# Kernel tuning notes

Measured on AMD Instinct MI355X. Metric: run time of the kernel, lower is better.

## Reference

```python
import jax, jax.numpy as jnp
import numpy as np
import math

EMBED_DIMS = 256
NUM_LANDMARKS = 40  # hard-coded k=40 in the original module
B, N = 2, 8192


def setup_inputs() -> dict:
    key = jax.random.key(0)
    ks = jax.random.split(key, 9)
    C = EMBED_DIMS
    w = lambda k: jax.random.normal(k, (C, C), dtype=jnp.float32) * 0.02
    b = lambda k: jax.random.normal(k, (C,), dtype=jnp.float32) * 0.02
    return {
        "query": jax.random.normal(ks[0], (B, N, C), dtype=jnp.float32),
        "Wq": w(ks[1]), "bq": b(ks[2]),
        "Wk": w(ks[3]), "bk": b(ks[4]),
        "Wv": w(ks[5]), "bv": b(ks[6]),
        "Wo": w(ks[7]), "bo": b(ks[8]),
    }


def reference(query, Wq, bq, Wk, bk, Wv, bv, Wo, bo):
    # key = value = identity = query (defaults in the original forward)
    C = query.shape[-1]
    scaling = math.sqrt(C)

    q = query @ Wq.T + bq  # [B, N, C]
    k = query @ Wk.T + bk
    v = query @ Wv.T + bv

    # Full similarity only to score keys: score_m[b, m] = sum_n sim_nm[b, n, m]
    sim_nm = jnp.einsum('bnc,bmc->bnm', q, k) / scaling  # [B, N, N]
    score_m = sim_nm.sum(axis=1)                          # [B, N]

    _, top_idx = jax.lax.top_k(score_m, NUM_LANDMARKS)    # [B, 40]
    selected = jnp.take_along_axis(k, top_idx[:, :, None], axis=1)  # [B, 40, C]

    sim_qn = jax.nn.softmax(jnp.einsum('bnc,bkc->bnk', q, selected) / scaling, axis=-1)  # [B, N, 40]
    sim_km = jax.nn.softmax(jnp.einsum('bmc,bkc->bmk', k, selected) / scaling, axis=-1)  # [B, N, 40]

    sim_qk = jnp.einsum('bnk,bmk->bnm', sim_qn, sim_km)   # [B, N, N]
    out = jnp.einsum('bnm,bmc->bnc', sim_qk, v)           # [B, N, C]
    out = out @ Wo.T + bo
    return query + out  # identity residual; dropouts are identity at p=0
```

## Files before the change

kernel.cpp:

```cpp
#include <hip/hip_runtime.h>
#include <cstddef>
#include <cstdint>

#define BATCH 2
#define SEQ 8192
#define CH 256
#define NLM 40
#define NLMP 48
#define MROWS (BATCH * SEQ)
#define INV_SCALE 0.0625f
#define NCBLK 256

typedef unsigned short ushort_t;
typedef __attribute__((ext_vector_type(8))) short short8;
typedef __attribute__((ext_vector_type(4))) float floatx4;

__device__ __forceinline__ ushort_t f2bf(float f) {
    unsigned int u = __float_as_uint(f);
    u += 0x7FFFu + ((u >> 16) & 1u);
    return (ushort_t)(u >> 16);
}
__device__ __forceinline__ float bf2f(ushort_t u) {
    return __uint_as_float(((unsigned)u) << 16);
}

__device__ __forceinline__ void gload_lds16(const ushort_t* g, ushort_t* l) {
    __builtin_amdgcn_global_load_lds(
        (const __attribute__((address_space(1))) unsigned int*)g,
        (__attribute__((address_space(3))) unsigned int*)l, 16, 0, 0);
}

__global__ __launch_bounds__(256) void convert_colsum(const float* __restrict__ x,
                                                      ushort_t* __restrict__ xbf,
                                                      float* __restrict__ partial) {
    __shared__ float red[4][256];
    const int b = blockIdx.y;
    const int r0 = blockIdx.x * 32;
    const int t = threadIdx.x;
    const int c4 = (t & 63) * 4;
    const int rg = t >> 6;
    const float* base = x + ((size_t)b * SEQ + r0) * 256;
    ushort_t* obase = xbf + ((size_t)b * SEQ + r0) * 256;
    float4 s = {0.f, 0.f, 0.f, 0.f};
#pragma unroll
    for (int i = 0; i < 8; i++) {
        const int r = rg + i * 4;
        const float4 a = *(const float4*)&base[(size_t)r * 256 + c4];
        uint2 o;
        o.x = f2bf(a.x) | ((unsigned)f2bf(a.y) << 16);
        o.y = f2bf(a.z) | ((unsigned)f2bf(a.w) << 16);
        *(uint2*)&obase[(size_t)r * 256 + c4] = o;
        s.x += a.x; s.y += a.y; s.z += a.z; s.w += a.w;
    }
    *(float4*)&red[rg][c4] = s;
    __syncthreads();
    const float tot = red[0][t] + red[1][t] + red[2][t] + red[3][t];
    partial[((size_t)b * NCBLK + blockIdx.x) * 256 + t] = tot;
}

__global__ __launch_bounds__(1024) void ws_kernel(const float* __restrict__ partial,
                                                  const float* __restrict__ Wq,
                                                  const float* __restrict__ bq,
                                                  const float* __restrict__ Wk,
                                                  float* __restrict__ ws,
                                                  float* __restrict__ tmat) {
    const int b = blockIdx.x;
    __shared__ float xs[256];
    __shared__ float qs[256];
    __shared__ float ppart[4][256];
    const int t = threadIdx.x;
    {
        float* tz = tmat + (size_t)b * NLM * 256;
        for (int i = t; i < NLM * 256; i += 1024) tz[i] = 0.f;
    }
    {
        const int c = t & 255, qd = t >> 8;
        const float* pb = partial + ((size_t)b * NCBLK + qd * 64) * 256 + c;
        float a = 0.f;
#pragma unroll 8
        for (int i = 0; i < 64; i++) a += pb[(size_t)i * 256];
        ppart[qd][c] = a;
    }
    __syncthreads();
    if (t < 256) xs[t] = ppart[0][t] + ppart[1][t] + ppart[2][t] + ppart[3][t];
    __syncthreads();
    const int lane = t & 63, w = t >> 6;
    {
        float4 wq[16];
#pragma unroll
        for (int g = 0; g < 16; g++)
            wq[g] = *(const float4*)&Wq[(size_t)(w * 16 + g) * 256 + lane * 4];
        const float4 x4 = *(const float4*)&xs[lane * 4];
#pragma unroll
        for (int g = 0; g < 16; g++) {
            const int o = w * 16 + g;
            float d = wq[g].x * x4.x + wq[g].y * x4.y + wq[g].z * x4.z + wq[g].w * x4.w;
#pragma unroll
            for (int off = 32; off >= 1; off >>= 1) d += __shfl_down(d, off);
            if (lane == 0) qs[o] = d + 8192.0f * bq[o];
        }
    }
    __syncthreads();
    const int c = t & 255, part = t >> 8;
    float a = 0.f;
#pragma unroll 16
    for (int o = part * 64; o < part * 64 + 64; o++)
        a += Wk[(size_t)o * 256 + c] * qs[o];
    ppart[part][c] = a;
    __syncthreads();
    if (t < 256)
        ws[b * 256 + t] = ppart[0][t] + ppart[1][t] + ppart[2][t] + ppart[3][t];
}

__global__ __launch_bounds__(256) void gemm_qkv_score(const ushort_t* __restrict__ xbf,
                                                      const float* __restrict__ Wq,
                                                      const float* __restrict__ Wk,
                                                      const float* __restrict__ Wv,
                                                      const float* __restrict__ bq,
                                                      const float* __restrict__ bk,
                                                      const float* __restrict__ bv,
                                                      ushort_t* __restrict__ qkv,
                                                      const float* __restrict__ query,
                                                      const float* __restrict__ ws,
                                                      float* __restrict__ score) {
    __shared__ __align__(16) char smem[24576];
    ushort_t* As = (ushort_t*)smem;
    ushort_t* Bs = (ushort_t*)(smem + 16384);
    ushort_t* Es = (ushort_t*)smem;
    const int z = blockIdx.z;
    const int t = threadIdx.x;
    const int lane = t & 63;
    const int w = t >> 6;

    if (z == 3) {
        const int blk = blockIdx.y * 4 + blockIdx.x;
#pragma unroll
        for (int i = 0; i < 8; i++) {
            const int g = blk * 32 + i * 4 + w;
            const int b = g >> 13;
            const int m = g & 8191;
            const float4 kv = *(const float4*)&query[(size_t)g * 256 + lane * 4];
            const float4 qs = *(const float4*)&ws[b * 256 + lane * 4];
            float d = kv.x * qs.x + kv.y * qs.y + kv.z * qs.z + kv.w * qs.w;
#pragma unroll
            for (int off = 32; off >= 1; off >>= 1) d += __shfl_down(d, off);
            if (lane == 0) score[(size_t)b * SEQ + m] = d * INV_SCALE;
        }
        return;
    }

    const float* __restrict__ W = (z == 0) ? Wq : (z == 1) ? Wk : Wv;
    const float* __restrict__ bias = (z == 0) ? bq : (z == 1) ? bk : bv;
    ushort_t* __restrict__ out = qkv + (size_t)z * MROWS * 256;
    const int o0 = blockIdx.x * 64;
    const int m0 = blockIdx.y * 128;
    const int quad = lane >> 4;
    const int l16 = lane & 15;
    const int xsw = l16 & 7;

    floatx4 acc[2][4];
#pragma unroll
    for (int rt = 0; rt < 2; rt++)
#pragma unroll
        for (int ct = 0; ct < 4; ct++) acc[rt][ct] = (floatx4){0.f, 0.f, 0.f, 0.f};

    for (int kc = 0; kc < 256; kc += 64) {
#pragma unroll
        for (int q = 0; q < 4; q++) {
            const int r0 = w * 32 + q * 8;
            gload_lds16(&xbf[(size_t)(m0 + r0 + (lane >> 3)) * 256 + kc +
                             (((lane & 7) ^ (lane >> 3)) * 8)],
                        &As[r0 * 64]);
        }
#pragma unroll
        for (int u = 0; u < 2; u++) {
            const int cid = t + u * 256;
            const int row = cid >> 3;
            const int cch = cid & 7;
            const float* wp = &W[(size_t)(o0 + row) * 256 + kc + cch * 8];
            const float4 a = *(const float4*)wp;
            const float4 c = *(const float4*)(wp + 4);
            uint4 o;
            o.x = f2bf(a.x) | ((unsigned)f2bf(a.y) << 16);
            o.y = f2bf(a.z) | ((unsigned)f2bf(a.w) << 16);
            o.z = f2bf(c.x) | ((unsigned)f2bf(c.y) << 16);
            o.w = f2bf(c.z) | ((unsigned)f2bf(c.w) << 16);
            *(uint4*)&Bs[row * 64 + ((cch ^ (row & 7)) * 8)] = o;
        }
        __syncthreads();
#pragma unroll
        for (int s = 0; s < 2; s++) {
            short8 a[2], bf[4];
#pragma unroll
            for (int rt = 0; rt < 2; rt++)
                a[rt] = *(const short8*)&As[(w * 32 + rt * 16 + l16) * 64 +
                                            (((s * 4 + quad) ^ xsw) * 8)];
#pragma unroll
            for (int ct = 0; ct < 4; ct++)
                bf[ct] = *(const short8*)&Bs[(ct * 16 + l16) * 64 +
                                             (((s * 4 + quad) ^ xsw) * 8)];
#pragma unroll
            for (int rt = 0; rt < 2; rt++)
#pragma unroll
                for (int ct = 0; ct < 4; ct++)
                    acc[rt][ct] = __builtin_amdgcn_mfma_f32_16x16x32_bf16(
                        a[rt], bf[ct], acc[rt][ct], 0, 0, 0);
        }
        __syncthreads();
    }

#pragma unroll
    for (int rt = 0; rt < 2; rt++) {
#pragma unroll
        for (int ct = 0; ct < 4; ct++) {
            const int col = ct * 16 + l16;
            const float bb = bias[o0 + col];
#pragma unroll
            for (int reg = 0; reg < 4; reg++) {
                const int row = w * 32 + rt * 16 + quad * 4 + reg;
                Es[row * 72 + col] = f2bf(acc[rt][ct][reg] + bb);
            }
        }
    }
    __syncthreads();
#pragma unroll
    for (int u = 0; u < 4; u++) {
        const int cid = t + u * 256;
        const int row = cid >> 3;
        const int off = (cid & 7) * 8;
        *(uint4*)&out[(size_t)(m0 + row) * 256 + o0 + off] =
            *(const uint4*)&Es[row * 72 + off];
    }
}

__global__ __launch_bounds__(1024) void topk_gather(const float* __restrict__ score,
                                                    const ushort_t* __restrict__ kmat,
                                                    ushort_t* __restrict__ sel) {
    const int b = blockIdx.x;
    const int t = threadIdx.x;
    __shared__ unsigned hist[256];
    __shared__ unsigned wsum[64];
    __shared__ unsigned sPrefix, sMask, sRem, sNeq;
    __shared__ int sNgt;
    __shared__ int top[NLM];
    __shared__ unsigned topkey[NLM];

    unsigned key[8];
#pragma unroll
    for (int j = 0; j < 8; j++) {
        const unsigned u = __float_as_uint(score[(size_t)b * SEQ + t + j * 1024]);
        key[j] = u ^ (unsigned)(((int)u >> 31) | 0x80000000);
    }
    if (t == 0) { sPrefix = 0; sMask = 0; sRem = NLM; sNgt = 0; sNeq = 0; }

    for (int lvl = 0; lvl < 4; lvl++) {
        const int shift = 24 - 8 * lvl;
        if (t < 256) hist[t] = 0;
        __syncthreads();
        const unsigned pfx = sPrefix, msk = sMask;
#pragma unroll
        for (int j = 0; j < 8; j++)
            if (((key[j] ^ pfx) & msk) == 0)
                atomicAdd(&hist[(key[j] >> shift) & 255u], 1u);
        __syncthreads();
        if (t < 64) wsum[t] = hist[t * 4] + hist[t * 4 + 1] + hist[t * 4 + 2] + hist[t * 4 + 3];
        __syncthreads();
        if (t == 0) {
            unsigned rem = sRem, cum = 0;
            int g = 63;
            for (; g > 0; g--) { if (cum + wsum[g] >= rem) break; cum += wsum[g]; }
            int d = g * 4 + 3;
            for (; d > g * 4; d--) { if (cum + hist[d] >= rem) break; cum += hist[d]; }
            sRem = rem - cum;
            sPrefix |= ((unsigned)d) << shift;
            sMask |= 255u << shift;
        }
        __syncthreads();
    }
    const unsigned K40 = sPrefix;
    const unsigned rem = sRem;
    const int ngt = NLM - (int)rem;

#pragma unroll
    for (int j = 0; j < 8; j++) {
        if (key[j] > K40) {
            const int slot = atomicAdd(&sNgt, 1);
            top[slot] = t + j * 1024; topkey[slot] = key[j];
        } else if (key[j] == K40) {
            const unsigned e = atomicAdd(&sNeq, 1u);
            if (e < rem) {
                const int slot = ngt + (int)e;
                top[slot] = t + j * 1024; topkey[slot] = key[j];
            }
        }
    }
    __syncthreads();

    if (t < 64) {
        unsigned long long c = (t < NLM)
            ? ((((unsigned long long)(~topkey[t])) << 32) | (unsigned)top[t])
            : 0xFFFFFFFFFFFFFFFFull;
#pragma unroll
        for (int kk = 2; kk <= 64; kk <<= 1) {
#pragma unroll
            for (int j = kk >> 1; j >= 1; j >>= 1) {
                const unsigned long long o = __shfl_xor(c, j);
                const bool takeMin = ((t & kk) == 0) == ((t & j) == 0);
                const bool less = c < o;
                c = (takeMin == less) ? c : o;
            }
        }
        if (t < NLM) top[t] = (int)(c & 0xFFFFFFFFu);
    }
    __syncthreads();

    for (int f = t; f < NLMP * 256; f += 1024) {
        const int j = f >> 8;
        const int cc = f & 255;
        sel[(size_t)b * NLMP * 256 + f] =
            (j < NLM) ? kmat[((size_t)b * SEQ + top[j]) * 256 + cc] : (ushort_t)0;
    }
}

__global__ __launch_bounds__(256, 4) void sim_fused(const ushort_t* __restrict__ qbf,
                                                    const ushort_t* __restrict__ kbf,
                                                    const ushort_t* __restrict__ vbf,
                                                    const ushort_t* __restrict__ sel,
                                                    float* __restrict__ simq,
                                                    float* __restrict__ tmat) {
    __shared__ __align__(16) char smem[43008];
    float (*Ps)[40]  = (float(*)[40])smem;
    ushort_t* Vs     = (ushort_t*)(smem + 10240);
    const int b = blockIdx.y;
    const int n0 = blockIdx.x * 64;
    const int t = threadIdx.x;
    const int lane = t & 63;
    const int w = t >> 6;
    const int quad = lane >> 4;
    const int l16 = lane & 15;
    const ushort_t* __restrict__ A = (blockIdx.z == 0) ? qbf : kbf;
    const ushort_t* __restrict__ Arow = A + ((size_t)b * SEQ + n0 + w * 16 + l16) * 256;
    const ushort_t* __restrict__ Sb = sel + (size_t)b * NLMP * 256 + (size_t)l16 * 256;

    floatx4 acc[3];
#pragma unroll
    for (int ct = 0; ct < 3; ct++) acc[ct] = (floatx4){0.f, 0.f, 0.f, 0.f};

#pragma unroll
    for (int ks = 0; ks < 8; ks++) {
        const int ko = ks * 32 + quad * 8;
        const short8 a  = *(const short8*)&Arow[ko];
        const short8 b0 = *(const short8*)&Sb[ko];
        const short8 b1 = *(const short8*)&Sb[16 * 256 + ko];
        const short8 b2 = *(const short8*)&Sb[32 * 256 + ko];
        acc[0] = __builtin_amdgcn_mfma_f32_16x16x32_bf16(a, b0, acc[0], 0, 0, 0);
        acc[1] = __builtin_amdgcn_mfma_f32_16x16x32_bf16(a, b1, acc[1], 0, 0, 0);
        acc[2] = __builtin_amdgcn_mfma_f32_16x16x32_bf16(a, b2, acc[2], 0, 0, 0);
    }

    const bool v2ok = (l16 < 8);
    float p0[4], p1[4], p2[4];
#pragma unroll
    for (int reg = 0; reg < 4; reg++) {
        const float l0 = acc[0][reg] * INV_SCALE;
        const float l1 = acc[1][reg] * INV_SCALE;
        const float l2 = acc[2][reg] * INV_SCALE;
        float m = fmaxf(l0, l1);
        if (v2ok) m = fmaxf(m, l2);
        m = fmaxf(m, __shfl_xor(m, 1));
        m = fmaxf(m, __shfl_xor(m, 2));
        m = fmaxf(m, __shfl_xor(m, 4));
        m = fmaxf(m, __shfl_xor(m, 8));
        const float e0 = expf(l0 - m);
        const float e1 = expf(l1 - m);
        const float e2 = v2ok ? expf(l2 - m) : 0.f;
        float s = e0 + e1 + e2;
        s += __shfl_xor(s, 1);
        s += __shfl_xor(s, 2);
        s += __shfl_xor(s, 4);
        s += __shfl_xor(s, 8);
        const float inv = 1.f / s;
        p0[reg] = e0 * inv; p1[reg] = e1 * inv; p2[reg] = e2 * inv;
    }

    const int row0 = w * 16 + quad * 4;
    if (blockIdx.z == 0) {
        float* __restrict__ dst = &simq[((size_t)b * SEQ + n0 + row0) * NLM];
#pragma unroll
        for (int reg = 0; reg < 4; reg++) {
            float* __restrict__ d2 = dst + reg * NLM;
            d2[l16] = p0[reg];
            d2[16 + l16] = p1[reg];
            if (v2ok) d2[32 + l16] = p2[reg];
        }
        return;
    }

#pragma unroll
    for (int reg = 0; reg < 4; reg++) {
        Ps[row0 + reg][l16] = p0[reg];
        Ps[row0 + reg][16 + l16] = p1[reg];
        if (v2ok) Ps[row0 + reg][32 + l16] = p2[reg];
    }
#pragma unroll
    for (int u = 0; u < 8; u++) {
        gload_lds16(&vbf[((size_t)b * SEQ + n0 + w * 2 + u * 8 + (lane >> 5)) * 256 +
                         (lane & 31) * 8],
                    &Vs[(w * 2 + u * 8) * 256]);
    }
    __syncthreads();

    float tac[40];
#pragma unroll
    for (int j = 0; j < 40; j++) tac[j] = 0.f;

#pragma unroll 2
    for (int m = 0; m < 64; m++) {
        const float vv = bf2f(Vs[m * 256 + t]);
#pragma unroll
        for (int j4 = 0; j4 < 10; j4++) {
            const float4 p = *(const float4*)&Ps[m][j4 * 4];
            tac[j4 * 4 + 0] = fmaf(p.x, vv, tac[j4 * 4 + 0]);
            tac[j4 * 4 + 1] = fmaf(p.y, vv, tac[j4 * 4 + 1]);
            tac[j4 * 4 + 2] = fmaf(p.z, vv, tac[j4 * 4 + 2]);
            tac[j4 * 4 + 3] = fmaf(p.w, vv, tac[j4 * 4 + 3]);
        }
    }
#pragma unroll
    for (int j = 0; j < 40; j++)
        atomicAdd(&tmat[(size_t)b * NLM * 256 + j * 256 + t], tac[j]);
}

__global__ __launch_bounds__(256) void out_pre_kernel(const float* __restrict__ simq,
                                                      const float* __restrict__ tmat,
                                                      ushort_t* __restrict__ outp_bf) {
    __shared__ float Pm[64][40];
    const int g0 = blockIdx.x * 64;
    const int b = g0 >> 13;
    const int t = threadIdx.x;
    float* pflat = &Pm[0][0];
    for (int f = t; f < 64 * NLM; f += 256) pflat[f] = simq[(size_t)g0 * NLM + f];
    float tc[40];
#pragma unroll
    for (int l = 0; l < 40; l++) tc[l] = tmat[(size_t)b * NLM * 256 + l * 256 + t];
    __syncthreads();
#pragma unroll 2
    for (int m = 0; m < 64; m++) {
        float a = 0.f;
#pragma unroll
        for (int j4 = 0; j4 < 10; j4++) {
            const float4 p = *(const float4*)&Pm[m][j4 * 4];
            a = fmaf(p.x, tc[j4 * 4 + 0], a);
            a = fmaf(p.y, tc[j4 * 4 + 1], a);
            a = fmaf(p.z, tc[j4 * 4 + 2], a);
            a = fmaf(p.w, tc[j4 * 4 + 3], a);
        }
        outp_bf[((size_t)g0 + m) * 256 + t] = f2bf(a);
    }
}

__global__ __launch_bounds__(256) void gemm_out(const ushort_t* __restrict__ Abf,
                                                const float* __restrict__ Wo,
                                                const float* __restrict__ bias,
                                                const float* __restrict__ resid,
                                                float* __restrict__ out) {
    __shared__ __align__(16) char smem[34816];
    ushort_t* As = (ushort_t*)smem;
    ushort_t* Bs = (ushort_t*)(smem + 16384);
    float* Ft = (float*)smem;
    const int t = threadIdx.x;
    const int o0 = blockIdx.x * 64;
    const int m0 = blockIdx.y * 128;
    const int lane = t & 63;
    const int w = t >> 6;
    const int quad = lane >> 4;
    const int l16 = lane & 15;
    const int xsw = l16 & 7;

    floatx4 acc[2][4];
#pragma unroll
    for (int rt = 0; rt < 2; rt++)
#pragma unroll
        for (int ct = 0; ct < 4; ct++) acc[rt][ct] = (floatx4){0.f, 0.f, 0.f, 0.f};

    for (int kc = 0; kc < 256; kc += 64) {
#pragma unroll
        for (int q = 0; q < 4; q++) {
            const int r0 = w * 32 + q * 8;
            gload_lds16(&Abf[(size_t)(m0 + r0 + (lane >> 3)) * 256 + kc +
                             (((lane & 7) ^ (lane >> 3)) * 8)],
                        &As[r0 * 64]);
        }
#pragma unroll
        for (int u = 0; u < 2; u++) {
            const int cid = t + u * 256;
            const int row = cid >> 3;
            const int cch = cid & 7;
            const float* wp = &Wo[(size_t)(o0 + row) * 256 + kc + cch * 8];
            const float4 a = *(const float4*)wp;
            const float4 c = *(const float4*)(wp + 4);
            uint4 o;
            o.x = f2bf(a.x) | ((unsigned)f2bf(a.y) << 16);
            o.y = f2bf(a.z) | ((unsigned)f2bf(a.w) << 16);
            o.z = f2bf(c.x) | ((unsigned)f2bf(c.y) << 16);
            o.w = f2bf(c.z) | ((unsigned)f2bf(c.w) << 16);
            *(uint4*)&Bs[row * 64 + ((cch ^ (row & 7)) * 8)] = o;
        }
        __syncthreads();
#pragma unroll
        for (int s = 0; s < 2; s++) {
            short8 a[2], bf[4];
#pragma unroll
            for (int rt = 0; rt < 2; rt++)
                a[rt] = *(const short8*)&As[(w * 32 + rt * 16 + l16) * 64 +
                                            (((s * 4 + quad) ^ xsw) * 8)];
#pragma unroll
            for (int ct = 0; ct < 4; ct++)
                bf[ct] = *(const short8*)&Bs[(ct * 16 + l16) * 64 +
                                             (((s * 4 + quad) ^ xsw) * 8)];
#pragma unroll
            for (int rt = 0; rt < 2; rt++)
#pragma unroll
                for (int ct = 0; ct < 4; ct++)
                    acc[rt][ct] = __builtin_amdgcn_mfma_f32_16x16x32_bf16(
                        a[rt], bf[ct], acc[rt][ct], 0, 0, 0);
        }
        __syncthreads();
    }

#pragma unroll
    for (int rt = 0; rt < 2; rt++) {
#pragma unroll
        for (int ct = 0; ct < 4; ct++) {
            const int col = ct * 16 + l16;
            const float bb = bias[o0 + col];
#pragma unroll
            for (int reg = 0; reg < 4; reg++) {
                const int row = w * 32 + rt * 16 + quad * 4 + reg;
                Ft[row * 68 + col] = acc[rt][ct][reg] + bb;
            }
        }
    }
    __syncthreads();
#pragma unroll
    for (int u = 0; u < 8; u++) {
        const int cid = t + u * 256;
        const int row = cid >> 4;
        const int off = (cid & 15) * 4;
        const float4 v = *(const float4*)&Ft[row * 68 + off];
        const float4 r4 = *(const float4*)&resid[(size_t)(m0 + row) * 256 + o0 + off];
        float4 o;
        o.x = v.x + r4.x; o.y = v.y + r4.y; o.z = v.z + r4.z; o.w = v.w + r4.w;
        *(float4*)&out[(size_t)(m0 + row) * 256 + o0 + off] = o;
    }
}

extern "C" void kernel_launch(void* const* d_in, const int* in_sizes, int n_in,
                              void* d_out, int out_size, void* d_ws, size_t ws_size,
                              hipStream_t stream) {
    const float* query = (const float*)d_in[0];
    const float* Wq = (const float*)d_in[1];
    const float* bq = (const float*)d_in[2];
    const float* Wk = (const float*)d_in[3];
    const float* bk = (const float*)d_in[4];
    const float* Wv = (const float*)d_in[5];
    const float* bv = (const float*)d_in[6];
    const float* Wo = (const float*)d_in[7];
    const float* bo = (const float*)d_in[8];
    float* out = (float*)d_out;

    char* p = (char*)d_ws;
    float* simq  = (float*)p;            p += (size_t)MROWS * NLM * 4;
    ushort_t* selbf = (ushort_t*)p;      p += (size_t)BATCH * NLMP * 256 * 2;
    float* tmat  = (float*)p;            p += (size_t)BATCH * NLM * 256 * 4;
    float* partial = (float*)p;          p += (size_t)BATCH * NCBLK * 256 * 4;
    float* ws    = (float*)p;            p += (size_t)BATCH * 256 * 4;
    float* score = (float*)p;            p += (size_t)BATCH * SEQ * 4;
    ushort_t* qkv = (ushort_t*)p;        p += (size_t)3 * MROWS * 256 * 2;
    ushort_t* xbf = (ushort_t*)p;        p += (size_t)MROWS * 256 * 2;
    ushort_t* qbf = qkv;
    ushort_t* kbf = qkv + (size_t)MROWS * 256;
    ushort_t* vbf = qkv + (size_t)2 * MROWS * 256;
    ushort_t* outp_bf = xbf;

    const dim3 blk(256);

    convert_colsum<<<dim3(SEQ / 32, BATCH), blk, 0, stream>>>(query, xbf, partial);
    ws_kernel<<<dim3(BATCH), dim3(1024), 0, stream>>>(partial, Wq, bq, Wk, ws, tmat);

    gemm_qkv_score<<<dim3(4, MROWS / 128, 4), blk, 0, stream>>>(
        xbf, Wq, Wk, Wv, bq, bk, bv, qkv, query, ws, score);

    topk_gather<<<dim3(BATCH), dim3(1024), 0, stream>>>(score, kbf, selbf);

    sim_fused<<<dim3(SEQ / 64, BATCH, 2), blk, 0, stream>>>(qbf, kbf, vbf, selbf, simq, tmat);

    out_pre_kernel<<<dim3(MROWS / 64), blk, 0, stream>>>(simq, tmat, outp_bf);
    gemm_out<<<dim3(4, MROWS / 128), blk, 0, stream>>>(outp_bf, Wo, bo, query, out);
}
```

Measured before the change: 188.1 us.

## Fuse out_pre into output GEMM and remap QKV grid for XCD locality

Merges the simq×tmat product into the output projection kernel, so the bf16 intermediate is built in shared memory per 64-row tile and is never written to or reread from global memory. Each 512-thread block covers all 256 output columns, which means the full Wo is converted to bf16 in every block. It also flattens the QKV GEMM grid to 1D with a remap that interleaves blocks across the 8 XCDs, aiming for better L2 locality. The costs are redundant Wo conversion per block, an epilogue that writes scattered non-vectorized stores, and tmat recompute per k-chunk.

New measurement: 185.2 us. No clear change (-1.6%).

```diff
diff --git a/kernel.cpp b/kernel.cpp
--- a/kernel.cpp
+++ b/kernel.cpp
@@ -127,13 +127,17 @@
     ushort_t* As = (ushort_t*)smem;
     ushort_t* Bs = (ushort_t*)(smem + 16384);
     ushort_t* Es = (ushort_t*)smem;
-    const int z = blockIdx.z;
+    const int lin = blockIdx.x;
+    const int wg = (lin & 7) * 256 + (lin >> 3);
+    const int bx = wg & 3;
+    const int by = (wg >> 2) & 127;
+    const int z = wg >> 9;
     const int t = threadIdx.x;
     const int lane = t & 63;
     const int w = t >> 6;
 
     if (z == 3) {
-        const int blk = blockIdx.y * 4 + blockIdx.x;
+        const int blk = by * 4 + bx;
 #pragma unroll
         for (int i = 0; i < 8; i++) {
             const int g = blk * 32 + i * 4 + w;
@@ -152,8 +156,8 @@
     const float* __restrict__ W = (z == 0) ? Wq : (z == 1) ? Wk : Wv;
     const float* __restrict__ bias = (z == 0) ? bq : (z == 1) ? bk : bv;
     ushort_t* __restrict__ out = qkv + (size_t)z * MROWS * 256;
-    const int o0 = blockIdx.x * 64;
-    const int m0 = blockIdx.y * 128;
+    const int o0 = bx * 64;
+    const int m0 = by * 128;
     const int quad = lane >> 4;
     const int l16 = lane & 15;
     const int xsw = l16 & 7;
@@ -431,72 +435,65 @@
         atomicAdd(&tmat[(size_t)b * NLM * 256 + j * 256 + t], tac[j]);
 }
 
-__global__ __launch_bounds__(256) void out_pre_kernel(const float* __restrict__ simq,
-                                                      const float* __restrict__ tmat,
-                                                      ushort_t* __restrict__ outp_bf) {
-    __shared__ float Pm[64][40];
-    const int g0 = blockIdx.x * 64;
-    const int b = g0 >> 13;
+__global__ __launch_bounds__(512) void out_fused(const float* __restrict__ simq,
+                                                 const float* __restrict__ tmat,
+                                                 const float* __restrict__ Wo,
+                                                 const float* __restrict__ bias,
+                                                 const float* __restrict__ resid,
+                                                 float* __restrict__ out) {
+    __shared__ __align__(16) char smem[51200];
+    float* Ps = (float*)smem;
+    ushort_t* Ac = (ushort_t*)(smem + 10240);
+    ushort_t* Bs = (ushort_t*)(smem + 18432);
+
     const int t = threadIdx.x;
-    float* pflat = &Pm[0][0];
-    for (int f = t; f < 64 * NLM; f += 256) pflat[f] = simq[(size_t)g0 * NLM + f];
-    float tc[40];
-#pragma unroll
-    for (int l = 0; l < 40; l++) tc[l] = tmat[(size_t)b * NLM * 256 + l * 256 + t];
-    __syncthreads();
-#pragma unroll 2
-    for (int m = 0; m < 64; m++) {
-        float a = 0.f;
-#pragma unroll
-        for (int j4 = 0; j4 < 10; j4++) {
-            const float4 p = *(const float4*)&Pm[m][j4 * 4];
-            a = fmaf(p.x, tc[j4 * 4 + 0], a);
-            a = fmaf(p.y, tc[j4 * 4 + 1], a);
-            a = fmaf(p.z, tc[j4 * 4 + 2], a);
-            a = fmaf(p.w, tc[j4 * 4 + 3], a);
-        }
-        outp_bf[((size_t)g0 + m) * 256 + t] = f2bf(a);
-    }
-}
-
-__global__ __launch_bounds__(256) void gemm_out(const ushort_t* __restrict__ Abf,
-                                                const float* __restrict__ Wo,
-                                                const float* __restrict__ bias,
-                                                const float* __restrict__ resid,
-                                                float* __restrict__ out) {
-    __shared__ __align__(16) char smem[34816];
-    ushort_t* As = (ushort_t*)smem;
-    ushort_t* Bs = (ushort_t*)(smem + 16384);
-    float* Ft = (float*)smem;
-    const int t = threadIdx.x;
-    const int o0 = blockIdx.x * 64;
-    const int m0 = blockIdx.y * 128;
+    const int m0 = blockIdx.x * 64;
+    const int b = blockIdx.x >> 7;
     const int lane = t & 63;
     const int w = t >> 6;
     const int quad = lane >> 4;
     const int l16 = lane & 15;
     const int xsw = l16 & 7;
-
-    floatx4 acc[2][4];
-#pragma unroll
-    for (int rt = 0; rt < 2; rt++)
-#pragma unroll
-        for (int ct = 0; ct < 4; ct++) acc[rt][ct] = (floatx4){0.f, 0.f, 0.f, 0.f};
+    const int rt_base = (w & 3) * 16;
+    const int cg_base = (w >> 2) * 8;
+
+    for (int f = t; f < 64 * NLM; f += 512)
+        Ps[f] = simq[(size_t)m0 * NLM + f];
+    __syncthreads();
+
+    floatx4 acc[8];
+#pragma unroll
+    for (int ct = 0; ct < 8; ct++) acc[ct] = (floatx4){0.f, 0.f, 0.f, 0.f};
+
+    const int kl = t & 63;
+    const int rg = t >> 6;
+    const float* __restrict__ Tb = tmat + (size_t)b * NLM * 256;
 
     for (int kc = 0; kc < 256; kc += 64) {
-#pragma unroll
-        for (int q = 0; q < 4; q++) {
-            const int r0 = w * 32 + q * 8;
-            gload_lds16(&Abf[(size_t)(m0 + r0 + (lane >> 3)) * 256 + kc +
-                             (((lane & 7) ^ (lane >> 3)) * 8)],
-                        &As[r0 * 64]);
-        }
-#pragma unroll
-        for (int u = 0; u < 2; u++) {
-            const int cid = t + u * 256;
+        {
+            float tc[40];
+#pragma unroll
+            for (int l = 0; l < 40; l++) tc[l] = Tb[l * 256 + kc + kl];
+#pragma unroll
+            for (int r = rg * 8; r < rg * 8 + 8; r++) {
+                float a = 0.f;
+#pragma unroll
+                for (int j4 = 0; j4 < 10; j4++) {
+                    const float4 p = *(const float4*)&Ps[r * 40 + j4 * 4];
+                    a = fmaf(p.x, tc[j4 * 4 + 0], a);
+                    a = fmaf(p.y, tc[j4 * 4 + 1], a);
+                    a = fmaf(p.z, tc[j4 * 4 + 2], a);
+                    a = fmaf(p.w, tc[j4 * 4 + 3], a);
+                }
+                Ac[r * 64 + (((kl >> 3) ^ (r & 7)) * 8) + (kl & 7)] = f2bf(a);
+            }
+        }
+#pragma unroll
+        for (int u = 0; u < 4; u++) {
+            const int cid = t + u * 512;
             const int row = cid >> 3;
             const int cch = cid & 7;
-            const float* wp = &Wo[(size_t)(o0 + row) * 256 + kc + cch * 8];
+            const float* wp = &Wo[(size_t)row * 256 + kc + cch * 8];
             const float4 a = *(const float4*)wp;
             const float4 c = *(const float4*)(wp + 4);
             uint4 o;
@@ -509,49 +506,28 @@
         __syncthreads();
 #pragma unroll
         for (int s = 0; s < 2; s++) {
-            short8 a[2], bf[4];
-#pragma unroll
-            for (int rt = 0; rt < 2; rt++)
-                a[rt] = *(const short8*)&As[(w * 32 + rt * 16 + l16) * 64 +
-                                            (((s * 4 + quad) ^ xsw) * 8)];
-#pragma unroll
-            for (int ct = 0; ct < 4; ct++)
-                bf[ct] = *(const short8*)&Bs[(ct * 16 + l16) * 64 +
-                                             (((s * 4 + quad) ^ xsw) * 8)];
-#pragma unroll
-            for (int rt = 0; rt < 2; rt++)
-#pragma unroll
-                for (int ct = 0; ct < 4; ct++)
-                    acc[rt][ct] = __builtin_amdgcn_mfma_f32_16x16x32_bf16(
-                        a[rt], bf[ct], acc[rt][ct], 0, 0, 0);
-        }
-        __syncthreads();
-    }
-
-#pragma unroll
-    for (int rt = 0; rt < 2; rt++) {
-#pragma unroll
-        for (int ct = 0; ct < 4; ct++) {
-            const int col = ct * 16 + l16;
-            const float bb = bias[o0 + col];
-#pragma unroll
-            for (int reg = 0; reg < 4; reg++) {
-                const int row = w * 32 + rt * 16 + quad * 4 + reg;
-                Ft[row * 68 + col] = acc[rt][ct][reg] + bb;
+            const short8 a = *(const short8*)&Ac[(rt_base + l16) * 64 +
+                                                 (((s * 4 + quad) ^ xsw) * 8)];
+#pragma unroll
+            for (int ct = 0; ct < 8; ct++) {
+                const short8 bf = *(const short8*)&Bs[((cg_base + ct) * 16 + l16) * 64 +
+                                                      (((s * 4 + quad) ^ xsw) * 8)];
+                acc[ct] = __builtin_amdgcn_mfma_f32_16x16x32_bf16(a, bf, acc[ct], 0, 0, 0);
             }
         }
-    }
-    __syncthreads();
-#pragma unroll
-    for (int u = 0; u < 8; u++) {
-        const int cid = t + u * 256;
-        const int row = cid >> 4;
-        const int off = (cid & 15) * 4;
-        const float4 v = *(const float4*)&Ft[row * 68 + off];
-        const float4 r4 = *(const float4*)&resid[(size_t)(m0 + row) * 256 + o0 + off];
-        float4 o;
-        o.x = v.x + r4.x; o.y = v.y + r4.y; o.z = v.z + r4.z; o.w = v.w + r4.w;
-        *(float4*)&out[(size_t)(m0 + row) * 256 + o0 + off] = o;
+        __syncthreads();
+    }
+
+#pragma unroll
+    for (int ct = 0; ct < 8; ct++) {
+        const int col = (cg_base + ct) * 16 + l16;
+        const float bb = bias[col];
+#pragma unroll
+        for (int reg = 0; reg < 4; reg++) {
+            const int row = rt_base + quad * 4 + reg;
+            const size_t idx = (size_t)(m0 + row) * 256 + col;
+            out[idx] = (acc[ct][reg] + bb) + resid[idx];
+        }
     }
 }
 
@@ -581,20 +557,18 @@
     ushort_t* qbf = qkv;
     ushort_t* kbf = qkv + (size_t)MROWS * 256;
     ushort_t* vbf = qkv + (size_t)2 * MROWS * 256;
-    ushort_t* outp_bf = xbf;
 
     const dim3 blk(256);
 
     convert_colsum<<<dim3(SEQ / 32, BATCH), blk, 0, stream>>>(query, xbf, partial);
     ws_kernel<<<dim3(BATCH), dim3(1024), 0, stream>>>(partial, Wq, bq, Wk, ws, tmat);
 
-    gemm_qkv_score<<<dim3(4, MROWS / 128, 4), blk, 0, stream>>>(
+    gemm_qkv_score<<<dim3(2048), blk, 0, stream>>>(
         xbf, Wq, Wk, Wv, bq, bk, bv, qkv, query, ws, score);
 
     topk_gather<<<dim3(BATCH), dim3(1024), 0, stream>>>(score, kbf, selbf);
 
     sim_fused<<<dim3(SEQ / 64, BATCH, 2), blk, 0, stream>>>(qbf, kbf, vbf, selbf, simq, tmat);
 
-    out_pre_kernel<<<dim3(MROWS / 64), blk, 0, stream>>>(simq, tmat, outp_bf);
-    gemm_out<<<dim3(4, MROWS / 128), blk, 0, stream>>>(outp_bf, Wo, bo, query, out);
-}
+    out_fused<<<dim3(MROWS / 64), dim3(512), 0, stream>>>(simq, tmat, Wo, bo, query, out);
+}
```
